# Kernel tuning notes

Measured on AMD Instinct MI355X. Metric: run time of the kernel, lower is better.

The kernel has to match this reference:

```python
import jax, jax.numpy as jnp
import numpy as np

B, S, T = 32, 48, 48
E_SRC, E_TRG, H, V = 512, 512, 1024, 32000


def setup_inputs() -> dict:
    key = jax.random.key(0)
    ks = jax.random.split(key, 18)
    stdv = 1.0 / np.sqrt(H)
    u = lambda k, shape, s: jax.random.uniform(k, shape, jnp.float32, -s, s)
    return {
        "input_src": jax.random.randint(ks[0], (B, S), 0, V),
        "input_trg": jax.random.randint(ks[1], (B, T), 0, V),
        "src_emb": u(ks[2], (V, E_SRC), 0.1),
        "trg_emb": u(ks[3], (V, E_TRG), 0.1),
        "enc_Wih": u(ks[4], (3 * H, E_SRC), stdv),
        "enc_Whh": u(ks[5], (3 * H, H), stdv),
        "enc_bih": u(ks[6], (3 * H,), stdv),
        "enc_bhh": u(ks[7], (3 * H,), stdv),
        "dec_Wi": u(ks[8], (3 * H, E_TRG), stdv),
        "dec_bi": u(ks[9], (3 * H,), stdv),
        "dec_Wh": u(ks[10], (3 * H, H), stdv),
        "dec_bh": u(ks[11], (3 * H,), stdv),
        "dec_Wp": u(ks[12], (3 * H, H), stdv),
        "dec_bp": u(ks[13], (3 * H,), stdv),
        "out_W": u(ks[14], (V, H), stdv),
        "out_b": jnp.zeros((V,), jnp.float32),
    }


def _encoder(x_emb, Wih, Whh, bih, bhh):
    # torch nn.GRU cell math, batch_first input [B,S,E]
    xg = jnp.einsum("bse,ge->bsg", x_emb, Wih) + bih  # [B,S,3H]
    h0 = jnp.zeros((x_emb.shape[0], H), x_emb.dtype)

    def step(h, xg_t):
        hg = h @ Whh.T + bhh
        xr, xz, xn = jnp.split(xg_t, 3, axis=-1)
        hr, hz, hn = jnp.split(hg, 3, axis=-1)
        r = jax.nn.sigmoid(xr + hr)
        z = jax.nn.sigmoid(xz + hz)
        n = jnp.tanh(xn + r * hn)
        h_new = (1.0 - z) * n + z * h
        return h_new, None

    h_last, _ = jax.lax.scan(step, h0, jnp.swapaxes(xg, 0, 1))
    return h_last  # [B,H]


def _cond_gru(y_emb, h0, ctx, Wi, bi, Wh, bh, Wp, bp):
    # ConditionalGRU with peephole on fixed ctx [B,H]
    ig = jnp.einsum("bte,ge->btg", y_emb, Wi) + bi  # [B,T,3H]
    pg = ctx @ Wp.T + bp  # [B,3H], constant over time
    pr, pz, pn = jnp.split(pg, 3, axis=-1)

    def step(h, ig_t):
        hg = h @ Wh.T + bh
        ir, iz, i_n = jnp.split(ig_t, 3, axis=-1)
        hr, hz, hn = jnp.split(hg, 3, axis=-1)
        resetgate = jax.nn.sigmoid(ir + hr + pr)
        inputgate = jax.nn.sigmoid(iz + hz + pz)
        newgate = jnp.tanh(i_n + resetgate * hn + pn)
        hy = newgate + inputgate * (h - newgate)
        return hy, hy

    _, hs = jax.lax.scan(step, h0, jnp.swapaxes(ig, 0, 1))
    return jnp.swapaxes(hs, 0, 1)  # [B,T,H]


def reference(input_src, input_trg, src_emb, trg_emb, enc_Wih, enc_Whh,
              enc_bih, enc_bhh, dec_Wi, dec_bi, dec_Wh, dec_bh, dec_Wp,
              dec_bp, out_W, out_b):
    x_emb = src_emb[input_src]                       # [B,S,E_src]
    h_t = _encoder(x_emb, enc_Wih, enc_Whh, enc_bih, enc_bhh)  # [B,H]
    y_emb = trg_emb[input_trg]                       # [B,T,E_trg]
    trg_h = _cond_gru(y_emb, h_t, h_t, dec_Wi, dec_bi, dec_Wh, dec_bh,
                      dec_Wp, dec_bp)                # [B,T,H]
    logits = jnp.einsum("bth,vh->btv", trg_h, out_W) + out_b  # [B,T,V]
    return logits
```

## Files before the change

### kernel.cpp

```cpp
#include <hip/hip_runtime.h>

#define DEV __device__ __forceinline__

typedef __bf16 bf16x8 __attribute__((ext_vector_type(8)));
typedef float f32x4 __attribute__((ext_vector_type(4)));

static constexpr int SL = 48;
static constexpr int HH = 1024;
static constexpr int G3 = 3072;

DEV float bf2f(unsigned short u){ unsigned int x = ((unsigned int)u) << 16; float f; __builtin_memcpy(&f,&x,4); return f; }
DEV unsigned short f2bf(float f){ unsigned int x; __builtin_memcpy(&x,&f,4); x = (x + 0x7fffu + ((x>>16)&1u)) >> 16; return (unsigned short)x; }
DEV float sigmf(float x){ return 1.0f/(1.0f + expf(-x)); }

DEV void gload16(const void* g, void* l){
  __builtin_amdgcn_global_load_lds((__attribute__((address_space(1))) void*)g,
                                   (__attribute__((address_space(3))) void*)l, 16, 0, 0);
}

__global__ void cvt_f32_bf16(const float* __restrict__ s, unsigned short* __restrict__ d, long n4){
  long i = blockIdx.x*(long)blockDim.x + threadIdx.x;
  const long stride = gridDim.x*(long)blockDim.x;
  for (; i < n4; i += stride){
    const float4 v = ((const float4*)s)[i];
    ushort4 o; o.x=f2bf(v.x); o.y=f2bf(v.y); o.z=f2bf(v.z); o.w=f2bf(v.w);
    ((ushort4*)d)[i] = o;
  }
}

__global__ void gather_cvt(const float* __restrict__ emb, const int* __restrict__ idx,
                           unsigned short* __restrict__ dst, int E){
  const int r = blockIdx.x;
  const int c = threadIdx.x * 4;
  const long row = idx[r];
  const float4 v = *(const float4*)(emb + row*(long)E + c);
  ushort4 o; o.x=f2bf(v.x); o.y=f2bf(v.y); o.z=f2bf(v.z); o.w=f2bf(v.w);
  *(ushort4*)(dst + (long)r*E + c) = o;
}

template<int OUTBF16>
__global__ __launch_bounds__(256, 2)
void gemm_bt(const unsigned short* __restrict__ A,
             const unsigned short* __restrict__ Bw,
             const float* __restrict__ bias,
             void* __restrict__ Cout,
             int N, int K)
{
  __shared__ unsigned short Alds[128*64];
  __shared__ unsigned short Blds[128*64];
  const int tid  = threadIdx.x;
  const int lane = tid & 63;
  const int wave = tid >> 6;
  const int tn = blockIdx.x, tm = blockIdx.y;
  const int wm = (wave >> 1) * 64, wn = (wave & 1) * 64;

  f32x4 acc[4][4] = {};

  const int srow = tid >> 3;
  const int scol = (tid & 7) * 8;

  for (int ks = 0; ks < K; ks += 64) {
    #pragma unroll
    for (int rd = 0; rd < 4; ++rd) {
      const int r = rd*32 + srow;
      gload16(A  + (long)(tm*128 + r)*(long)K + ks + scol, &Alds[r*64 + scol]);
      gload16(Bw + (long)(tn*128 + r)*(long)K + ks + scol, &Blds[r*64 + scol]);
    }
    __syncthreads();
    #pragma unroll
    for (int kk = 0; kk < 2; ++kk) {
      bf16x8 af[4], bq[4];
      #pragma unroll
      for (int i=0;i<4;i++)
        af[i] = *(const bf16x8*)&Alds[(wm + i*16 + (lane&15))*64 + kk*32 + (lane>>4)*8];
      #pragma unroll
      for (int j=0;j<4;j++)
        bq[j] = *(const bf16x8*)&Blds[(wn + j*16 + (lane&15))*64 + kk*32 + (lane>>4)*8];
      #pragma unroll
      for (int i=0;i<4;i++)
        #pragma unroll
        for (int j=0;j<4;j++)
          acc[i][j] = __builtin_amdgcn_mfma_f32_16x16x32_bf16(af[i], bq[j], acc[i][j], 0,0,0);
    }
    __syncthreads();
  }

  const int c0 = lane & 15;
  const int r0 = (lane >> 4) * 4;
  #pragma unroll
  for (int j=0;j<4;j++){
    const int gcol = tn*128 + wn + j*16 + c0;
    const float bv = bias[gcol];
    #pragma unroll
    for (int i=0;i<4;i++){
      const long rowb = (long)(tm*128 + wm + i*16 + r0);
      #pragma unroll
      for (int r=0;r<4;r++){
        const float v = acc[i][j][r] + bv;
        const long off = (rowb + r)*(long)N + gcol;
        if (OUTBF16) ((unsigned short*)Cout)[off] = f2bf(v);
        else         ((float*)Cout)[off] = v;
      }
    }
  }
}


DEV int wswz(int row, int kbyte){ return (row*2048 + kbyte) ^ ((row & 7) << 4); }

DEV void load_w(char* WldsB, const unsigned short* Wsrc, int wg, int tid){
  for (int ch = tid; ch < 6144; ch += 256) {
    const int row = ch >> 7;
    const int kb  = (ch & 127) << 4;
    const int g = row >> 4, wr = row & 15;
    const char* src = (const char*)Wsrc + ((long)(g*HH + wg*16 + wr))*2048 + kb;
    *(uint4*)(WldsB + wswz(row, kb)) = *(const uint4*)src;
  }
}

DEV void step_gemm(const char* WldsB, const unsigned short* ch,
                   float* hgp, int lane, int wave)
{
  const int mt = wave & 1, kh = wave >> 1;
  const unsigned short* ah = ch + (mt*16 + (lane&15))*HH + kh*512 + (lane>>4)*8;
  const int rr0 = lane & 15;
  const int kb0 = kh*1024 + (lane>>4)*16;
  f32x4 a0 = {0.f,0.f,0.f,0.f}; f32x4 a1 = a0, a2 = a0;
  #pragma unroll
  for (int kk=0; kk<16; ++kk) {
    const bf16x8 av = *(const bf16x8*)(ah + kk*32);
    const bf16x8 b0 = *(const bf16x8*)(WldsB + wswz(rr0,      kb0 + kk*64));
    const bf16x8 b1 = *(const bf16x8*)(WldsB + wswz(rr0 + 16, kb0 + kk*64));
    const bf16x8 b2 = *(const bf16x8*)(WldsB + wswz(rr0 + 32, kb0 + kk*64));
    a0 = __builtin_amdgcn_mfma_f32_16x16x32_bf16(av, b0, a0, 0,0,0);
    a1 = __builtin_amdgcn_mfma_f32_16x16x32_bf16(av, b1, a1, 0,0,0);
    a2 = __builtin_amdgcn_mfma_f32_16x16x32_bf16(av, b2, a2, 0,0,0);
  }
  const int bb = mt*16 + (lane>>4)*4;
  #pragma unroll
  for (int r=0;r<4;r++){
    hgp[((kh*3+0)*32 + bb + r)*16 + rr0] = a0[r];
    hgp[((kh*3+1)*32 + bb + r)*16 + rr0] = a1[r];
    hgp[((kh*3+2)*32 + bb + r)*16 + rr0] = a2[r];
  }
}

DEV void pg_gemm(const unsigned short* Wp, const unsigned short* ch,
                 float* hgp, int wg, int lane, int wave)
{
  const int mt = wave & 1, kh = wave >> 1;
  const unsigned short* ah = ch + (mt*16 + (lane&15))*HH + kh*512 + (lane>>4)*8;
  const unsigned short* w0 = Wp + ((long)(0*HH + wg*16 + (lane&15)))*HH + kh*512 + (lane>>4)*8;
  const unsigned short* w1 = Wp + ((long)(1*HH + wg*16 + (lane&15)))*HH + kh*512 + (lane>>4)*8;
  const unsigned short* w2 = Wp + ((long)(2*HH + wg*16 + (lane&15)))*HH + kh*512 + (lane>>4)*8;
  f32x4 a0 = {0.f,0.f,0.f,0.f}; f32x4 a1 = a0, a2 = a0;
  #pragma unroll
  for (int kk=0; kk<16; ++kk) {
    const bf16x8 av = *(const bf16x8*)(ah + kk*32);
    const bf16x8 b0 = *(const bf16x8*)(w0 + kk*32);
    const bf16x8 b1 = *(const bf16x8*)(w1 + kk*32);
    const bf16x8 b2 = *(const bf16x8*)(w2 + kk*32);
    a0 = __builtin_amdgcn_mfma_f32_16x16x32_bf16(av, b0, a0, 0,0,0);
    a1 = __builtin_amdgcn_mfma_f32_16x16x32_bf16(av, b1, a1, 0,0,0);
    a2 = __builtin_amdgcn_mfma_f32_16x16x32_bf16(av, b2, a2, 0,0,0);
  }
  const int rr0 = lane & 15;
  const int bb = mt*16 + (lane>>4)*4;
  #pragma unroll
  for (int r=0;r<4;r++){
    hgp[((kh*3+0)*32 + bb + r)*16 + rr0] = a0[r];
    hgp[((kh*3+1)*32 + bb + r)*16 + rr0] = a1[r];
    hgp[((kh*3+2)*32 + bb + r)*16 + rr0] = a2[r];
  }
}

DEV void grid_barrier(unsigned* slots, unsigned& id, int wg, int tid)
{
  const unsigned my = ++id;
  __syncthreads();
  if (tid == 0)
    __hip_atomic_store(&slots[wg*32], my, __ATOMIC_RELEASE, __HIP_MEMORY_SCOPE_AGENT);
  if (tid < 64) {
    int guard = 0;
    while (__hip_atomic_load(&slots[tid*32], __ATOMIC_RELAXED, __HIP_MEMORY_SCOPE_AGENT) < my) {
      __builtin_amdgcn_s_sleep(1);
      if (++guard > 4000000) break;
    }
    __threadfence();
  }
  __syncthreads();
}

__global__ __launch_bounds__(256, 1)
void scan_kernel(const unsigned short* __restrict__ Whh, const float* __restrict__ bhh,
                 const unsigned short* __restrict__ Wh,  const float* __restrict__ bh,
                 const unsigned short* __restrict__ Wp,  const float* __restrict__ bp,
                 const unsigned short* __restrict__ xg, const unsigned short* __restrict__ ig,
                 unsigned short* h0, unsigned short* h1,
                 unsigned short* trg_h,
                 unsigned* slots)
{
  extern __shared__ char smem[];
  char*  WldsB = smem;
  float* hgp   = (float*)(smem + 98304);
  float* pgl   = (float*)(smem + 110592);
  float* biasl = (float*)(smem + 116736);

  const int tid = threadIdx.x, wg = blockIdx.x;
  const int lane = tid & 63, wave = tid >> 6;
  unsigned barid = 0;
  float hreg[2] = {0.f, 0.f};

  load_w(WldsB, Whh, wg, tid);
  if (tid < 48) biasl[tid] = bhh[(tid>>4)*HH + wg*16 + (tid&15)];
  __syncthreads();

  #pragma unroll 1
  for (int s = 0; s < SL; ++s) {
    const unsigned short* ch = (s & 1) ? h1 : h0;
    unsigned short* nh = (s & 1) ? h0 : h1;
    step_gemm(WldsB, ch, hgp, lane, wave);
    __syncthreads();
    #pragma unroll
    for (int u = 0; u < 2; ++u) {
      const int e = tid + u*256;
      const int b = e >> 4, c = e & 15;
      const unsigned short* xrow = xg + (long)(b*SL + s)*G3 + wg*16 + c;
      const float hr = hgp[e]        + hgp[1536 + e] + biasl[c];
      const float hz = hgp[512 + e]  + hgp[2048 + e] + biasl[16 + c];
      const float hn = hgp[1024 + e] + hgp[2560 + e] + biasl[32 + c];
      const float rg = sigmf(bf2f(xrow[0]) + hr);
      const float zg = sigmf(bf2f(xrow[1024]) + hz);
      const float ng = tanhf(bf2f(xrow[2048]) + rg*hn);
      const float hN = (1.f - zg)*ng + zg*hreg[u];
      hreg[u] = hN;
      nh[b*HH + wg*16 + c] = f2bf(hN);
    }
    grid_barrier(slots, barid, wg, tid);
  }

  pg_gemm(Wp, h0, hgp, wg, lane, wave);
  __syncthreads();
  #pragma unroll
  for (int u = 0; u < 2; ++u) {
    const int e = tid + u*256;
    const int c = e & 15;
    #pragma unroll
    for (int g = 0; g < 3; ++g)
      pgl[g*512 + e] = hgp[g*512 + e] + hgp[(3+g)*512 + e] + bp[g*HH + wg*16 + c];
  }
  __syncthreads();
  load_w(WldsB, Wh, wg, tid);
  if (tid < 48) biasl[tid] = bh[(tid>>4)*HH + wg*16 + (tid&15)];
  __syncthreads();

  #pragma unroll 1
  for (int t = 0; t < SL; ++t) {
    const unsigned short* ch = (t & 1) ? h1 : h0;
    unsigned short* nh = (t & 1) ? h0 : h1;
    step_gemm(WldsB, ch, hgp, lane, wave);
    __syncthreads();
    #pragma unroll
    for (int u = 0; u < 2; ++u) {
      const int e = tid + u*256;
      const int b = e >> 4, c = e & 15;
      const unsigned short* irow = ig + (long)(b*SL + t)*G3 + wg*16 + c;
      const float hr = hgp[e]        + hgp[1536 + e] + biasl[c]      + pgl[e];
      const float hz = hgp[512 + e]  + hgp[2048 + e] + biasl[16 + c] + pgl[512 + e];
      const float hn = hgp[1024 + e] + hgp[2560 + e] + biasl[32 + c];
      const float rg = sigmf(bf2f(irow[0]) + hr);
      const float zg = sigmf(bf2f(irow[1024]) + hz);
      const float ng = tanhf(bf2f(irow[2048]) + rg*hn + pgl[1024 + e]);
      const float hN = ng + zg*(hreg[u] - ng);
      hreg[u] = hN;
      const unsigned short hv = f2bf(hN);
      trg_h[(long)(b*SL + t)*HH + wg*16 + c] = hv;
      nh[b*HH + wg*16 + c] = hv;
    }
    if (t != SL-1) grid_barrier(slots, barid, wg, tid);
  }
}

extern "C" void kernel_launch(void* const* d_in, const int* in_sizes, int n_in,
                              void* d_out, int out_size, void* d_ws, size_t ws_size,
                              hipStream_t stream)
{
  (void)in_sizes; (void)n_in; (void)out_size; (void)ws_size;
  const int*   input_src = (const int*)d_in[0];
  const int*   input_trg = (const int*)d_in[1];
  const float* src_emb = (const float*)d_in[2];
  const float* trg_emb = (const float*)d_in[3];
  const float* enc_Wih = (const float*)d_in[4];
  const float* enc_Whh = (const float*)d_in[5];
  const float* enc_bih = (const float*)d_in[6];
  const float* enc_bhh = (const float*)d_in[7];
  const float* dec_Wi  = (const float*)d_in[8];
  const float* dec_bi  = (const float*)d_in[9];
  const float* dec_Wh  = (const float*)d_in[10];
  const float* dec_bh  = (const float*)d_in[11];
  const float* dec_Wp  = (const float*)d_in[12];
  const float* dec_bp  = (const float*)d_in[13];
  const float* out_W   = (const float*)d_in[14];
  const float* out_b   = (const float*)d_in[15];

  char* ws = (char*)d_ws;
  unsigned short* b16 = (unsigned short*)d_ws;
  unsigned* slots = (unsigned*)ws;
  unsigned short* h0     = (unsigned short*)(ws + 8192);
  unsigned short* h1     = (unsigned short*)(ws + 73728);
  unsigned short* trg_h  = (unsigned short*)(ws + 139264);
  unsigned short* A_src  = (unsigned short*)(ws + 3284992);
  unsigned short* A_trg  = (unsigned short*)(ws + 4857856);
  unsigned short* Wih_b  = (unsigned short*)(ws + 6430720);
  unsigned short* Wi_b   = (unsigned short*)(ws + 9576448);
  unsigned short* Whh_b  = (unsigned short*)(ws + 12722176);
  unsigned short* Wh_b   = (unsigned short*)(ws + 19013632);
  unsigned short* Wp_b   = (unsigned short*)(ws + 25305088);
  unsigned short* outW_b = (unsigned short*)(ws + 31596544);
  unsigned short* xg     = (unsigned short*)(ws + 97132544);
  unsigned short* ig     = (unsigned short*)(ws + 106569728);
  (void)b16;

  hipMemsetAsync(d_ws, 0, 73728, stream);

  gather_cvt<<<1536, 128, 0, stream>>>(src_emb, input_src, A_src, 512);
  gather_cvt<<<1536, 128, 0, stream>>>(trg_emb, input_trg, A_trg, 512);
  auto cvt = [&](const float* s, unsigned short* d, long n){
    long n4 = n >> 2;
    int grid = (int)((n4 + 255) >> 8); if (grid > 2048) grid = 2048;
    cvt_f32_bf16<<<grid, 256, 0, stream>>>(s, d, n4);
  };
  cvt(enc_Wih, Wih_b, 3072L*512);
  cvt(dec_Wi,  Wi_b,  3072L*512);
  cvt(enc_Whh, Whh_b, 3072L*1024);
  cvt(dec_Wh,  Wh_b,  3072L*1024);
  cvt(dec_Wp,  Wp_b,  3072L*1024);
  cvt(out_W,   outW_b, 32000L*1024);

  gemm_bt<1><<<dim3(24,12), 256, 0, stream>>>(A_src, Wih_b, enc_bih, xg, 3072, 512);
  gemm_bt<1><<<dim3(24,12), 256, 0, stream>>>(A_trg, Wi_b,  dec_bi,  ig, 3072, 512);

  constexpr int kSmem = 116928;
  (void)hipFuncSetAttribute(reinterpret_cast<const void*>(scan_kernel),
                            hipFuncAttributeMaxDynamicSharedMemorySize, kSmem);
  scan_kernel<<<64, 256, kSmem, stream>>>(Whh_b, enc_bhh, Wh_b, dec_bh, Wp_b, dec_bp,
                                          xg, ig, h0, h1, trg_h, slots);

  gemm_bt<0><<<dim3(250,12), 256, 0, stream>>>(trg_h, outW_b, out_b, d_out, 32000, 1024);
}
```

Measured before the change: 1.344 ms.

## Replace fenced grid barrier with cache-bypassing h loads/stores and relaxed flags

The hidden state exchanged between workgroups is now written and read with sc0 sc1 global instructions, which bypass the non-coherent caches. This lets the grid barrier drop its release ordering and __threadfence in favour of a plain vmcnt wait. The step GEMM prefetches all 16 h fragments up front before the MFMA loop. The gate epilogue is remapped so each thread handles two adjacent columns with packed 32-bit loads and stores, and the last decoder step skips the unneeded h write. Correctness now rests on hand-written memory ordering through inline asm instead of the documented HIP atomics semantics.

Result: faster. 1.123 ms (-16.4%).

```diff
diff --git a/kernel.cpp b/kernel.cpp
--- a/kernel.cpp
+++ b/kernel.cpp
@@ -4,6 +4,7 @@
 
 typedef __bf16 bf16x8 __attribute__((ext_vector_type(8)));
 typedef float f32x4 __attribute__((ext_vector_type(4)));
+typedef unsigned int u32x4 __attribute__((ext_vector_type(4)));
 
 static constexpr int SL = 48;
 static constexpr int HH = 1024;
@@ -16,6 +17,15 @@
 DEV void gload16(const void* g, void* l){
   __builtin_amdgcn_global_load_lds((__attribute__((address_space(1))) void*)g,
                                    (__attribute__((address_space(3))) void*)l, 16, 0, 0);
+}
+
+DEV u32x4 ld16_sc1(const void* p){
+  u32x4 r;
+  asm volatile("global_load_dwordx4 %0, %1, off sc0 sc1" : "=&v"(r) : "v"(p));
+  return r;
+}
+DEV void st4_sc1(void* p, unsigned v){
+  asm volatile("global_store_dword %0, %1, off sc0 sc1" :: "v"(p), "v"(v) : "memory");
 }
 
 __global__ void cvt_f32_bf16(const float* __restrict__ s, unsigned short* __restrict__ d, long n4){
@@ -123,12 +133,18 @@
 {
   const int mt = wave & 1, kh = wave >> 1;
   const unsigned short* ah = ch + (mt*16 + (lane&15))*HH + kh*512 + (lane>>4)*8;
+  u32x4 hv[16];
+  #pragma unroll
+  for (int kk=0; kk<16; ++kk) hv[kk] = ld16_sc1(ah + kk*32);
+  asm volatile("s_waitcnt vmcnt(0)" ::: "memory");
+  __builtin_amdgcn_sched_barrier(0);
+
   const int rr0 = lane & 15;
   const int kb0 = kh*1024 + (lane>>4)*16;
   f32x4 a0 = {0.f,0.f,0.f,0.f}; f32x4 a1 = a0, a2 = a0;
   #pragma unroll
   for (int kk=0; kk<16; ++kk) {
-    const bf16x8 av = *(const bf16x8*)(ah + kk*32);
+    bf16x8 av; __builtin_memcpy(&av, &hv[kk], 16);
     const bf16x8 b0 = *(const bf16x8*)(WldsB + wswz(rr0,      kb0 + kk*64));
     const bf16x8 b1 = *(const bf16x8*)(WldsB + wswz(rr0 + 16, kb0 + kk*64));
     const bf16x8 b2 = *(const bf16x8*)(WldsB + wswz(rr0 + 32, kb0 + kk*64));
@@ -153,10 +169,15 @@
   const unsigned short* w0 = Wp + ((long)(0*HH + wg*16 + (lane&15)))*HH + kh*512 + (lane>>4)*8;
   const unsigned short* w1 = Wp + ((long)(1*HH + wg*16 + (lane&15)))*HH + kh*512 + (lane>>4)*8;
   const unsigned short* w2 = Wp + ((long)(2*HH + wg*16 + (lane&15)))*HH + kh*512 + (lane>>4)*8;
+  u32x4 hv[16];
+  #pragma unroll
+  for (int kk=0; kk<16; ++kk) hv[kk] = ld16_sc1(ah + kk*32);
+  asm volatile("s_waitcnt vmcnt(0)" ::: "memory");
+  __builtin_amdgcn_sched_barrier(0);
   f32x4 a0 = {0.f,0.f,0.f,0.f}; f32x4 a1 = a0, a2 = a0;
   #pragma unroll
   for (int kk=0; kk<16; ++kk) {
-    const bf16x8 av = *(const bf16x8*)(ah + kk*32);
+    bf16x8 av; __builtin_memcpy(&av, &hv[kk], 16);
     const bf16x8 b0 = *(const bf16x8*)(w0 + kk*32);
     const bf16x8 b1 = *(const bf16x8*)(w1 + kk*32);
     const bf16x8 b2 = *(const bf16x8*)(w2 + kk*32);
@@ -177,16 +198,16 @@
 DEV void grid_barrier(unsigned* slots, unsigned& id, int wg, int tid)
 {
   const unsigned my = ++id;
+  asm volatile("s_waitcnt vmcnt(0)" ::: "memory");
   __syncthreads();
   if (tid == 0)
-    __hip_atomic_store(&slots[wg*32], my, __ATOMIC_RELEASE, __HIP_MEMORY_SCOPE_AGENT);
+    __hip_atomic_store(&slots[wg*32], my, __ATOMIC_RELAXED, __HIP_MEMORY_SCOPE_AGENT);
   if (tid < 64) {
     int guard = 0;
     while (__hip_atomic_load(&slots[tid*32], __ATOMIC_RELAXED, __HIP_MEMORY_SCOPE_AGENT) < my) {
       __builtin_amdgcn_s_sleep(1);
       if (++guard > 4000000) break;
     }
-    __threadfence();
   }
   __syncthreads();
 }
@@ -209,6 +230,10 @@
   const int tid = threadIdx.x, wg = blockIdx.x;
   const int lane = tid & 63, wave = tid >> 6;
   unsigned barid = 0;
+
+  const int pb = tid >> 3;
+  const int pc = (tid & 7) * 2;
+  const int e0 = pb*16 + pc;
   float hreg[2] = {0.f, 0.f};
 
   load_w(WldsB, Whh, wg, tid);
@@ -221,20 +246,26 @@
     unsigned short* nh = (s & 1) ? h0 : h1;
     step_gemm(WldsB, ch, hgp, lane, wave);
     __syncthreads();
-    #pragma unroll
-    for (int u = 0; u < 2; ++u) {
-      const int e = tid + u*256;
-      const int b = e >> 4, c = e & 15;
-      const unsigned short* xrow = xg + (long)(b*SL + s)*G3 + wg*16 + c;
-      const float hr = hgp[e]        + hgp[1536 + e] + biasl[c];
-      const float hz = hgp[512 + e]  + hgp[2048 + e] + biasl[16 + c];
-      const float hn = hgp[1024 + e] + hgp[2560 + e] + biasl[32 + c];
-      const float rg = sigmf(bf2f(xrow[0]) + hr);
-      const float zg = sigmf(bf2f(xrow[1024]) + hz);
-      const float ng = tanhf(bf2f(xrow[2048]) + rg*hn);
-      const float hN = (1.f - zg)*ng + zg*hreg[u];
-      hreg[u] = hN;
-      nh[b*HH + wg*16 + c] = f2bf(hN);
+    {
+      const unsigned short* xrow = xg + (long)(pb*SL + s)*G3 + wg*16 + pc;
+      const unsigned xr = *(const unsigned*)(xrow);
+      const unsigned xz = *(const unsigned*)(xrow + 1024);
+      const unsigned xn = *(const unsigned*)(xrow + 2048);
+      unsigned packed = 0;
+      #pragma unroll
+      for (int j = 0; j < 2; ++j) {
+        const int e = e0 + j, c = pc + j;
+        const float hr = hgp[e]        + hgp[1536 + e] + biasl[c];
+        const float hz = hgp[512 + e]  + hgp[2048 + e] + biasl[16 + c];
+        const float hn = hgp[1024 + e] + hgp[2560 + e] + biasl[32 + c];
+        const float rg = sigmf(bf2f((unsigned short)(xr >> (16*j))) + hr);
+        const float zg = sigmf(bf2f((unsigned short)(xz >> (16*j))) + hz);
+        const float ng = tanhf(bf2f((unsigned short)(xn >> (16*j))) + rg*hn);
+        const float hN = (1.f - zg)*ng + zg*hreg[j];
+        hreg[j] = hN;
+        packed |= ((unsigned)f2bf(hN)) << (16*j);
+      }
+      st4_sc1(nh + pb*HH + wg*16 + pc, packed);
     }
     grid_barrier(slots, barid, wg, tid);
   }
@@ -242,9 +273,8 @@
   pg_gemm(Wp, h0, hgp, wg, lane, wave);
   __syncthreads();
   #pragma unroll
-  for (int u = 0; u < 2; ++u) {
-    const int e = tid + u*256;
-    const int c = e & 15;
+  for (int j = 0; j < 2; ++j) {
+    const int e = e0 + j, c = pc + j;
     #pragma unroll
     for (int g = 0; g < 3; ++g)
       pgl[g*512 + e] = hgp[g*512 + e] + hgp[(3+g)*512 + e] + bp[g*HH + wg*16 + c];
@@ -260,22 +290,27 @@
     unsigned short* nh = (t & 1) ? h0 : h1;
     step_gemm(WldsB, ch, hgp, lane, wave);
     __syncthreads();
-    #pragma unroll
-    for (int u = 0; u < 2; ++u) {
-      const int e = tid + u*256;
-      const int b = e >> 4, c = e & 15;
-      const unsigned short* irow = ig + (long)(b*SL + t)*G3 + wg*16 + c;
-      const float hr = hgp[e]        + hgp[1536 + e] + biasl[c]      + pgl[e];
-      const float hz = hgp[512 + e]  + hgp[2048 + e] + biasl[16 + c] + pgl[512 + e];
-      const float hn = hgp[1024 + e] + hgp[2560 + e] + biasl[32 + c];
-      const float rg = sigmf(bf2f(irow[0]) + hr);
-      const float zg = sigmf(bf2f(irow[1024]) + hz);
-      const float ng = tanhf(bf2f(irow[2048]) + rg*hn + pgl[1024 + e]);
-      const float hN = ng + zg*(hreg[u] - ng);
-      hreg[u] = hN;
-      const unsigned short hv = f2bf(hN);
-      trg_h[(long)(b*SL + t)*HH + wg*16 + c] = hv;
-      nh[b*HH + wg*16 + c] = hv;
+    {
+      const unsigned short* irow = ig + (long)(pb*SL + t)*G3 + wg*16 + pc;
+      const unsigned xr = *(const unsigned*)(irow);
+      const unsigned xz = *(const unsigned*)(irow + 1024);
+      const unsigned xn = *(const unsigned*)(irow + 2048);
+      unsigned packed = 0;
+      #pragma unroll
+      for (int j = 0; j < 2; ++j) {
+        const int e = e0 + j, c = pc + j;
+        const float hr = hgp[e]        + hgp[1536 + e] + biasl[c]      + pgl[e];
+        const float hz = hgp[512 + e]  + hgp[2048 + e] + biasl[16 + c] + pgl[512 + e];
+        const float hn = hgp[1024 + e] + hgp[2560 + e] + biasl[32 + c];
+        const float rg = sigmf(bf2f((unsigned short)(xr >> (16*j))) + hr);
+        const float zg = sigmf(bf2f((unsigned short)(xz >> (16*j))) + hz);
+        const float ng = tanhf(bf2f((unsigned short)(xn >> (16*j))) + rg*hn + pgl[1024 + e]);
+        const float hN = ng + zg*(hreg[j] - ng);
+        hreg[j] = hN;
+        packed |= ((unsigned)f2bf(hN)) << (16*j);
+      }
+      *(unsigned*)(trg_h + (long)(pb*SL + t)*HH + wg*16 + pc) = packed;
+      if (t != SL-1) st4_sc1(nh + pb*HH + wg*16 + pc, packed);
     }
     if (t != SL-1) grid_barrier(slots, barid, wg, tid);
   }
@@ -304,7 +339,6 @@
   const float* out_b   = (const float*)d_in[15];
 
   char* ws = (char*)d_ws;
-  unsigned short* b16 = (unsigned short*)d_ws;
   unsigned* slots = (unsigned*)ws;
   unsigned short* h0     = (unsigned short*)(ws + 8192);
   unsigned short* h1     = (unsigned short*)(ws + 73728);
@@ -319,7 +353,6 @@
   unsigned short* outW_b = (unsigned short*)(ws + 31596544);
   unsigned short* xg     = (unsigned short*)(ws + 97132544);
   unsigned short* ig     = (unsigned short*)(ws + 106569728);
-  (void)b16;
 
   hipMemsetAsync(d_ws, 0, 73728, stream);
 
```
